# Performance work log

Measured on AMD Instinct MI355X. Metric: run time of the kernel, lower is better.

## Reference

```python
import jax, jax.numpy as jnp
import numpy as np

WH, WW, NUM_HEADS = 7, 7, 16
DIM = 512
B_WINDOWS = 4096   # batch * num_windows
NW = 64            # num_windows per image (mask groups)
N = WH * WW        # 49 tokens per window


def _relative_position_index():
    # Mirrors the torch buffer construction exactly (torch.meshgrid default is 'ij').
    coords = np.stack(np.meshgrid(np.arange(WH), np.arange(WW), indexing='ij'))  # [2,WH,WW]
    cf = coords.reshape(2, -1)                              # [2, N]
    rel = cf[:, :, None] - cf[:, None, :]                   # [2, N, N]
    rel = rel.transpose(1, 2, 0).copy()                     # [N, N, 2]
    rel[:, :, 0] += WH - 1
    rel[:, :, 1] += WW - 1
    rel[:, :, 0] *= 2 * WW - 1
    return jnp.asarray(rel.sum(-1), dtype=jnp.int32)        # [N, N]

REL_IDX = _relative_position_index()


def setup_inputs() -> dict:
    key = jax.random.key(0)
    ks = jax.random.split(key, 7)
    return {
        'x':          jax.random.normal(ks[0], (B_WINDOWS, N, DIM), jnp.float32),
        'mask':       jax.random.normal(ks[1], (NW, N, N), jnp.float32),
        'Wqkv':       jax.random.normal(ks[2], (3 * DIM, DIM), jnp.float32) * (DIM ** -0.5),
        'bqkv':       jax.random.normal(ks[3], (3 * DIM,), jnp.float32) * 0.02,
        'bias_table': jax.random.normal(ks[4], ((2 * WH - 1) * (2 * WW - 1), NUM_HEADS), jnp.float32) * 0.02,
        'Wproj':      jax.random.normal(ks[5], (DIM, DIM), jnp.float32) * (DIM ** -0.5),
        'bproj':      jax.random.normal(ks[6], (DIM,), jnp.float32) * 0.02,
    }


def reference(x, mask, Wqkv, bqkv, bias_table, Wproj, bproj):
    B, n, C = x.shape                      # [B_, 49, 512]
    hd = C // NUM_HEADS
    scale = hd ** -0.5
    qkv = (x @ Wqkv.T + bqkv).reshape(B, n, 3, NUM_HEADS, hd)
    qkv = qkv.transpose(2, 0, 3, 1, 4)     # [3, B, H, N, hd]
    q, k, v = qkv[0] * scale, qkv[1], qkv[2]
    attn = jnp.einsum('bhnd,bhmd->bhnm', q, k)          # [B, H, N, N]
    # gathered relative position bias: [1, H, N, N]
    bias = bias_table[REL_IDX].transpose(2, 0, 1)[None]
    attn = attn + bias
    nW = mask.shape[0]
    attn = attn.reshape(B // nW, nW, NUM_HEADS, n, n) + mask[None, :, None]
    attn = jax.nn.softmax(attn.reshape(B, NUM_HEADS, n, n), axis=-1)
    out = jnp.einsum('bhnm,bhmd->bhnd', attn, v)        # [B, H, N, hd]
    out = out.transpose(0, 2, 1, 3).reshape(B, n, C)
    return out @ Wproj.T + bproj
```

## Files before the change

kernel.cpp:

```cpp
#include <hip/hip_runtime.h>
#include <stdint.h>

#define NHEADS 16
#define DIM 512
#define BWIN 4096
#define NTOK 49
#define M_TOTAL (BWIN * NTOK)
#define QSCALE 0.17677669529663687f

typedef __attribute__((ext_vector_type(4)))  float f32x4;
typedef __attribute__((ext_vector_type(16))) float f32x16;
typedef __attribute__((ext_vector_type(8)))  short s16x8;
typedef __attribute__((ext_vector_type(4)))  short s16x4;

__device__ __forceinline__ f32x4 mfma16(s16x8 a, s16x8 b, f32x4 c) {
    return __builtin_amdgcn_mfma_f32_16x16x32_bf16(a, b, c, 0, 0, 0);
}
__device__ __forceinline__ f32x16 mfma32(s16x8 a, s16x8 b, f32x16 c) {
    return __builtin_amdgcn_mfma_f32_32x32x16_bf16(a, b, c, 0, 0, 0);
}

__device__ __forceinline__ short f2bf(float f) {
    unsigned u = __builtin_bit_cast(unsigned, f);
    u += 0x7FFFu + ((u >> 16) & 1u);
    return (short)(u >> 16);
}

__device__ __forceinline__ unsigned cvtpk(float a, float b) {
    unsigned r;
    asm("v_cvt_pk_bf16_f32 %0, %1, %2" : "=v"(r) : "v"(a), "v"(b));
    return r;
}

__device__ __forceinline__ void gload16(const void* g, void* l) {
    __builtin_amdgcn_global_load_lds(
        (const __attribute__((address_space(1))) void*)g,
        (__attribute__((address_space(3))) void*)l, 16, 0, 0);
}


__global__ void k_prep_x(const float* __restrict__ x, short* __restrict__ xb) {
    int i = blockIdx.x * blockDim.x + threadIdx.x;
    int stride = gridDim.x * blockDim.x;
    const int n4 = M_TOTAL * DIM / 4;
    for (; i < n4; i += stride) {
        f32x4 v = ((const f32x4*)x)[i];
        s16x4 o;
        o[0] = f2bf(v[0]); o[1] = f2bf(v[1]); o[2] = f2bf(v[2]); o[3] = f2bf(v[3]);
        ((s16x4*)xb)[i] = o;
    }
}

__global__ void k_prep_w(const float* __restrict__ src, short* __restrict__ dst,
                         int n, int scale_lim) {
    int i = blockIdx.x * blockDim.x + threadIdx.x;
    int stride = gridDim.x * blockDim.x;
    for (; i < n; i += stride) {
        float v = src[i];
        if (i < scale_lim) v *= QSCALE;
        dst[i] = f2bf(v);
    }
}

__global__ void k_prep_bm(const float* __restrict__ btab, const float* __restrict__ mask,
                          float* __restrict__ bmT) {
    int idx = blockIdx.x * blockDim.x + threadIdx.x;
    int stride = gridDim.x * blockDim.x;
    const int n = 64 * NHEADS * 49 * 64;
    for (; idx < n; idx += stride) {
        int i = idx & 63;
        int rest = idx >> 6;
        int j = rest % 49;
        int wh = rest / 49;
        int head = wh & 15;
        int w64 = wh >> 4;
        float v = 0.f;
        if (i < 49) {
            int ridx = (i / 7 - j / 7 + 6) * 13 + (i % 7 - j % 7 + 6);
            v = btab[ridx * 16 + head] + mask[(w64 * 49 + i) * 49 + j];
        }
        bmT[idx] = v;
    }
}

template <int MODE>
__global__ __launch_bounds__(512, 2) void k_gemm(
    const short* __restrict__ A, const short* __restrict__ B,
    const float* __restrict__ bias, void* __restrict__ C,
    int ntiles, int nwg) {
    __shared__ short lA[2][256 * 64];
    __shared__ short lB[2][256 * 64];
    const int K = 512;
    const size_t MP = M_TOTAL;

    int bid   = blockIdx.x;
    int chunk = nwg >> 3;
    int wg    = (bid & 7) * chunk + (bid >> 3);
    int mt = wg / ntiles;
    int nt = wg - mt * ntiles;

    int t = threadIdx.x;
    int lane = t & 63, wid = t >> 6;
    int l15 = lane & 15, g = (lane >> 4) & 3;
    int wr = wid >> 2, wc = wid & 3;

    const short* aT = A + (size_t)mt * 256 * K;
    const short* bT = B + (size_t)nt * 256 * K;

    f32x4 acc[8][4] = {};
    s16x8 af[4][2], bf0[2][2], bf1[2][2];

#define STAGE_A(buf, H, kt) do {                                               \
    _Pragma("unroll") for (int j = 0; j < 2; j++) {                            \
        int r_ = j * 128 + (H) * 64 + (t >> 3);                                \
        int sc_ = (t & 7) ^ (r_ & 7);                                          \
        gload16(aT + (size_t)r_ * K + (kt) * 64 + sc_ * 8,                     \
                &lA[buf][r_ * 64 + (t & 7) * 8]);                              \
    } } while (0)

#define STAGE_B(buf, H, kt) do {                                               \
    _Pragma("unroll") for (int j = 0; j < 2; j++) {                            \
        int u_ = j * 64 + (t >> 3);                                            \
        int r_ = ((u_ >> 5) << 6) | ((H) << 5) | (u_ & 31);                    \
        int sc_ = (t & 7) ^ (r_ & 7);                                          \
        gload16(bT + (size_t)r_ * K + (kt) * 64 + sc_ * 8,                     \
                &lB[buf][r_ * 64 + (t & 7) * 8]);                              \
    } } while (0)

#define LDA(MH, cur) do {                                                      \
    const short* pa_ = &lA[cur][(wr * 128 + (MH) * 64 + l15) * 64];            \
    _Pragma("unroll") for (int mi = 0; mi < 4; mi++)                           \
    _Pragma("unroll") for (int ks = 0; ks < 2; ks++)                           \
        af[mi][ks] = *(const s16x8*)(pa_ + mi * 1024 +                         \
                                     (((ks * 4 + g) ^ (l15 & 7)) * 8));        \
    } while (0)

#define LDB(BF, NH, cur) do {                                                  \
    const short* pb_ = &lB[cur][(wc * 64 + (NH) * 32 + l15) * 64];             \
    _Pragma("unroll") for (int nj = 0; nj < 2; nj++)                           \
    _Pragma("unroll") for (int ks = 0; ks < 2; ks++)                           \
        BF[nj][ks] = *(const s16x8*)(pb_ + nj * 1024 +                         \
                                     (((ks * 4 + g) ^ (l15 & 7)) * 8));        \
    } while (0)

#define MMQ(BF, MH, NH) do {                                                   \
    __builtin_amdgcn_s_setprio(1);                                             \
    _Pragma("unroll") for (int ks = 0; ks < 2; ks++)                           \
    _Pragma("unroll") for (int mi = 0; mi < 4; mi++)                           \
    _Pragma("unroll") for (int nj = 0; nj < 2; nj++)                           \
        acc[(MH) * 4 + mi][(NH) * 2 + nj] =                                    \
            mfma16(af[mi][ks], BF[nj][ks], acc[(MH) * 4 + mi][(NH) * 2 + nj]); \
    __builtin_amdgcn_s_setprio(0);                                             \
} while (0)

#define BAR() __builtin_amdgcn_s_barrier()
#define LGW() do { asm volatile("s_waitcnt lgkmcnt(0)" ::: "memory");          \
                   __builtin_amdgcn_sched_barrier(0); } while (0)
#define VMW(st) do {                                                           \
    if (st) asm volatile("s_waitcnt vmcnt(4)" ::: "memory");                   \
    else    asm volatile("s_waitcnt vmcnt(0)" ::: "memory"); } while (0)

    STAGE_A(0, 0, 0);
    STAGE_B(0, 0, 0);
    STAGE_B(0, 1, 0);
    STAGE_A(0, 1, 0);
    asm volatile("s_waitcnt vmcnt(4)" ::: "memory");
    BAR();

    for (int kt = 0; kt < 8; ++kt) {
        const int cur = kt & 1, nxt = cur ^ 1;
        const bool st = kt < 7;
        LDA(0, cur); LDB(bf0, 0, cur);
        if (st) STAGE_A(nxt, 0, kt + 1);
        VMW(st); BAR(); LGW();
        MMQ(bf0, 0, 0);
        BAR();
        LDB(bf1, 1, cur);
        if (st) STAGE_B(nxt, 0, kt + 1);
        VMW(st); BAR(); LGW();
        MMQ(bf1, 0, 1);
        BAR();
        LDA(1, cur);
        if (st) STAGE_B(nxt, 1, kt + 1);
        VMW(st); BAR(); LGW();
        MMQ(bf1, 1, 1);
        BAR();
        if (st) STAGE_A(nxt, 1, kt + 1);
        VMW(st); BAR(); LGW();
        MMQ(bf0, 1, 0);
        BAR();
    }

#undef STAGE_A
#undef STAGE_B
#undef LDA
#undef LDB
#undef MMQ
#undef BAR
#undef LGW
#undef VMW

    int m0 = mt * 256 + wr * 128;
    int n0 = nt * 256 + wc * 64;

    if (MODE == 0) {
        short* region = (wid < 4) ? (&lA[0][0] + wid * 8192)
                                  : (&lB[0][0] + (wid - 4) * 8192);
#pragma unroll
        for (int a = 0; a < 4; a++) {
            int co = (a >> 1) * 32 + (a & 1) * 16;
            int n = n0 + co + l15;
            float bv = bias[n];
            if (n < 512) bv *= QSCALE;
            int w16 = (co >> 3) + (l15 >> 3);
#pragma unroll
            for (int mi = 0; mi < 8; mi++)
#pragma unroll
                for (int r = 0; r < 4; r++) {
                    int row = mi * 16 + g * 4 + r;
                    region[row * 64 + ((w16 ^ (row & 7)) * 8) + (l15 & 7)] =
                        f2bf(acc[mi][a][r] + bv);
                }
        }
#pragma unroll
        for (int p = 0; p < 2; p++) {
            int plane = (n0 >> 5) + p;
            short* dst = (short*)C + ((size_t)plane * MP + m0) * 32;
#pragma unroll
            for (int i = 0; i < 8; i++) {
                int f = i * 64 + lane;
                int row = f >> 2, c = f & 3;
                s16x8 v = *(const s16x8*)(region + row * 64 +
                                          (((p * 4 + c) ^ (row & 7)) * 8));
                *(s16x8*)(dst + (size_t)f * 8) = v;
            }
        }
    } else {
#pragma unroll
        for (int a = 0; a < 4; a++) {
            int co = (a >> 1) * 32 + (a & 1) * 16;
            int n = n0 + co + l15;
            float bv = bias[n];
#pragma unroll
            for (int mi = 0; mi < 8; mi++)
#pragma unroll
                for (int r = 0; r < 4; r++) {
                    int m = m0 + mi * 16 + g * 4 + r;
                    ((float*)C)[(size_t)m * 512 + n] = acc[mi][a][r] + bv;
                }
        }
    }
}

__global__ __launch_bounds__(256, 4) void k_attn(
    const short* __restrict__ qkv, const float* __restrict__ bmT,
    short* __restrict__ ao) {
    int wid = threadIdx.x >> 6, lane = threadIdx.x & 63;
    int p = blockIdx.x * 4 + wid;
    int w = p >> 4, head = p & 15;
    int l31 = lane & 31, h = lane >> 5;
    const size_t MP = M_TOTAL;

    const short* qb = qkv + ((size_t)head * MP + w * 49) * 32;
    const short* kb = qb + (size_t)16 * MP * 32;
    const short* vb = qb + (size_t)32 * MP * 32;

    s16x8 qf[2][2], kf[2][2];
#pragma unroll
    for (int t = 0; t < 2; t++) {
        int row = t * 32 + l31;
#pragma unroll
        for (int s = 0; s < 2; s++) {
            qf[t][s] = *(const s16x8*)(qb + row * 32 + 16 * s + 8 * h);
            kf[t][s] = *(const s16x8*)(kb + row * 32 + 16 * s + 8 * h);
        }
    }

    union U8 { short s[8]; s16x8 v; };
    U8 vf[4];
#pragma unroll
    for (int jc = 0; jc < 4; jc++)
#pragma unroll
        for (int e = 0; e < 8; e++)
            vf[jc].s[e] = vb[(16 * jc + 8 * h + e) * 32 + l31];

    f32x16 st[2][2] = {};
#pragma unroll
    for (int s = 0; s < 2; s++)
#pragma unroll
        for (int jt = 0; jt < 2; jt++)
#pragma unroll
            for (int it = 0; it < 2; it++)
                st[jt][it] = mfma32(kf[jt][s], qf[it][s], st[jt][it]);

    const float* bs = bmT + ((size_t)((w & 63) * NHEADS + head)) * 3136 + l31;
#pragma unroll
    for (int jt = 0; jt < 2; jt++)
#pragma unroll
        for (int it = 0; it < 2; it++)
#pragma unroll
            for (int r = 0; r < 16; r++) {
                int j = 32 * jt + (r & 3) + 8 * (r >> 2) + 4 * h;
                if (j < 49) st[jt][it][r] += bs[j * 64 + 32 * it];
                else        st[jt][it][r] = -1e30f;
            }

    float inv[2];
#pragma unroll
    for (int it = 0; it < 2; it++) {
        float mx = -1e30f;
#pragma unroll
        for (int jt = 0; jt < 2; jt++)
#pragma unroll
            for (int r = 0; r < 16; r++) mx = fmaxf(mx, st[jt][it][r]);
        mx = fmaxf(mx, __shfl_xor(mx, 32));
        float sum = 0.f;
#pragma unroll
        for (int jt = 0; jt < 2; jt++)
#pragma unroll
            for (int r = 0; r < 16; r++) {
                float e = __expf(st[jt][it][r] - mx);
                st[jt][it][r] = e;
                sum += e;
            }
        sum += __shfl_xor(sum, 32);
        inv[it] = 1.0f / sum;
    }

    f32x16 oacc[2] = {};
#pragma unroll
    for (int jc = 0; jc < 4; jc++) {
        const int jt = jc >> 1, rb = 8 * (jc & 1);
#pragma unroll
        for (int it = 0; it < 2; it++) {
            float iv = inv[it];
            unsigned pk0  = cvtpk(st[jt][it][rb + 0] * iv, st[jt][it][rb + 1] * iv);
            unsigned pk0b = cvtpk(st[jt][it][rb + 2] * iv, st[jt][it][rb + 3] * iv);
            unsigned pk1  = cvtpk(st[jt][it][rb + 4] * iv, st[jt][it][rb + 5] * iv);
            unsigned pk1b = cvtpk(st[jt][it][rb + 6] * iv, st[jt][it][rb + 7] * iv);
            unsigned o0  = __shfl_xor(pk0, 32);
            unsigned o0b = __shfl_xor(pk0b, 32);
            unsigned o1  = __shfl_xor(pk1, 32);
            unsigned o1b = __shfl_xor(pk1b, 32);
            union { unsigned d[4]; s16x8 v; } pa;
            pa.d[0] = h ? o1  : pk0;
            pa.d[1] = h ? o1b : pk0b;
            pa.d[2] = h ? pk1 : o0;
            pa.d[3] = h ? pk1b : o0b;
            oacc[it] = mfma32(pa.v, vf[jc].v, oacc[it]);
        }
    }

    short* ob = ao + (size_t)w * 49 * 512 + head * 32 + l31;
#pragma unroll
    for (int it = 0; it < 2; it++)
#pragma unroll
        for (int r = 0; r < 16; r++) {
            int i = 32 * it + 4 * h + (r & 3) + 8 * (r >> 2);
            if (i < 49) ob[(size_t)i * 512] = f2bf(oacc[it][r]);
        }
}


extern "C" void kernel_launch(void* const* d_in, const int* in_sizes, int n_in,
                              void* d_out, int out_size, void* d_ws, size_t ws_size,
                              hipStream_t stream) {
    const float* x     = (const float*)d_in[0];
    const float* mask  = (const float*)d_in[1];
    const float* Wqkv  = (const float*)d_in[2];
    const float* bqkv  = (const float*)d_in[3];
    const float* btab  = (const float*)d_in[4];
    const float* Wproj = (const float*)d_in[5];
    const float* bproj = (const float*)d_in[6];
    float* out = (float*)d_out;

    char* ws = (char*)d_ws;
    size_t off = 0;
    short* xb     = (short*)(ws + off); off += (size_t)M_TOTAL * 512 * 2;
    short* qkvb   = (short*)(ws + off); off += (size_t)48 * M_TOTAL * 32 * 2 + 65536;
    short* Wqkvb  = (short*)(ws + off); off += (size_t)1536 * 512 * 2;
    short* Wprojb = (short*)(ws + off); off += (size_t)512 * 512 * 2;
    float* bmT    = (float*)(ws + off); off += (size_t)64 * NHEADS * 49 * 64 * 4;
    short* ao = xb;

    k_prep_x<<<2048, 256, 0, stream>>>(x, xb);
    k_prep_w<<<1536, 256, 0, stream>>>(Wqkv, Wqkvb, 1536 * 512, 512 * 512);
    k_prep_w<<<512, 256, 0, stream>>>(Wproj, Wprojb, 512 * 512, 0);
    k_prep_bm<<<2048, 256, 0, stream>>>(btab, mask, bmT);

    k_gemm<0><<<4704, 512, 0, stream>>>(xb, Wqkvb, bqkv, qkvb, 6, 4704);
    k_attn<<<16384, 256, 0, stream>>>(qkvb, bmT, ao);
    k_gemm<1><<<1568, 512, 0, stream>>>(ao, Wprojb, bproj, out, 2, 1568);
}
```

Before: 1.164 ms.

## Deepen GEMM global-to-LDS prefetch pipeline and peel final k-iteration

Restructures the double-buffered K loop so the A half-tile for iteration kt+2 is staged into the current buffer after its last use, keeping more global loads in flight (vmcnt 6 instead of 4). The last iteration is peeled into an epilogue with progressively draining waits, which removes the per-iteration conditional staging. This aims to hide more global memory latency behind MFMA work, at the cost of more complex buffer-reuse ordering and more outstanding loads.

```diff
diff --git a/kernel.cpp b/kernel.cpp
--- a/kernel.cpp
+++ b/kernel.cpp
@@ -156,37 +156,57 @@
 #define BAR() __builtin_amdgcn_s_barrier()
 #define LGW() do { asm volatile("s_waitcnt lgkmcnt(0)" ::: "memory");          \
                    __builtin_amdgcn_sched_barrier(0); } while (0)
-#define VMW(st) do {                                                           \
-    if (st) asm volatile("s_waitcnt vmcnt(4)" ::: "memory");                   \
-    else    asm volatile("s_waitcnt vmcnt(0)" ::: "memory"); } while (0)
+#define VMW(n) asm volatile("s_waitcnt vmcnt(" #n ")" ::: "memory")
 
     STAGE_A(0, 0, 0);
     STAGE_B(0, 0, 0);
     STAGE_B(0, 1, 0);
     STAGE_A(0, 1, 0);
-    asm volatile("s_waitcnt vmcnt(4)" ::: "memory");
+    STAGE_A(1, 0, 1);
+    VMW(6);
     BAR();
 
-    for (int kt = 0; kt < 8; ++kt) {
+    for (int kt = 0; kt < 7; ++kt) {
         const int cur = kt & 1, nxt = cur ^ 1;
-        const bool st = kt < 7;
         LDA(0, cur); LDB(bf0, 0, cur);
-        if (st) STAGE_A(nxt, 0, kt + 1);
-        VMW(st); BAR(); LGW();
+        STAGE_B(nxt, 0, kt + 1);
+        VMW(6); BAR(); LGW();
         MMQ(bf0, 0, 0);
         BAR();
         LDB(bf1, 1, cur);
-        if (st) STAGE_B(nxt, 0, kt + 1);
-        VMW(st); BAR(); LGW();
+        STAGE_B(nxt, 1, kt + 1);
+        VMW(6); BAR(); LGW();
         MMQ(bf1, 0, 1);
         BAR();
         LDA(1, cur);
-        if (st) STAGE_B(nxt, 1, kt + 1);
-        VMW(st); BAR(); LGW();
+        STAGE_A(nxt, 1, kt + 1);
+        VMW(6); BAR(); LGW();
         MMQ(bf1, 1, 1);
         BAR();
-        if (st) STAGE_A(nxt, 1, kt + 1);
-        VMW(st); BAR(); LGW();
+        if (kt < 6) {
+            STAGE_A(cur, 0, kt + 2);
+            VMW(6);
+        } else {
+            VMW(4);
+        }
+        BAR(); LGW();
+        MMQ(bf0, 1, 0);
+        BAR();
+    }
+    {
+        LDA(0, 1); LDB(bf0, 0, 1);
+        VMW(2); BAR(); LGW();
+        MMQ(bf0, 0, 0);
+        BAR();
+        LDB(bf1, 1, 1);
+        VMW(0); BAR(); LGW();
+        MMQ(bf1, 0, 1);
+        BAR();
+        LDA(1, 1);
+        BAR(); LGW();
+        MMQ(bf1, 1, 1);
+        BAR();
+        LGW();
         MMQ(bf0, 1, 0);
         BAR();
     }
```

After: 1.174 ms. No clear change (+0.9%).

## Double-buffer A fragments and prefetch next tile's A from LDS during MFMA

Applied to the files above, without the earlier changes.

Reworks the GEMM main loop so it keeps two register sets of A fragments and a single B fragment set. The next k-tile's A fragments are read from LDS while the current MFMAs run, using partial lgkmcnt waits (lgkmcnt(8)) instead of full drains. Global-to-LDS staging is regrouped, with explicit vmcnt counts tuned to the new issue order. The aim is to hide LDS read latency behind matrix work. In exchange it uses more registers, reloads the B fragments an extra time per iteration, and depends on hand-counted wait values being correct.

```diff
diff --git a/kernel.cpp b/kernel.cpp
--- a/kernel.cpp
+++ b/kernel.cpp
@@ -108,7 +108,7 @@
     const short* bT = B + (size_t)nt * 256 * K;
 
     f32x4 acc[8][4] = {};
-    s16x8 af[4][2], bf0[2][2], bf1[2][2];
+    s16x8 afA[4][2], afB[4][2], S[2][2];
 
 #define STAGE_A(buf, H, kt) do {                                               \
     _Pragma("unroll") for (int j = 0; j < 2; j++) {                            \
@@ -127,77 +127,90 @@
                 &lB[buf][r_ * 64 + (t & 7) * 8]);                              \
     } } while (0)
 
-#define LDA(MH, cur) do {                                                      \
-    const short* pa_ = &lA[cur][(wr * 128 + (MH) * 64 + l15) * 64];            \
+#define LDAF(DST, MH, buf) do {                                                \
+    const short* pa_ = &lA[buf][(wr * 128 + (MH) * 64 + l15) * 64];            \
     _Pragma("unroll") for (int mi = 0; mi < 4; mi++)                           \
     _Pragma("unroll") for (int ks = 0; ks < 2; ks++)                           \
-        af[mi][ks] = *(const s16x8*)(pa_ + mi * 1024 +                         \
-                                     (((ks * 4 + g) ^ (l15 & 7)) * 8));        \
+        DST[mi][ks] = *(const s16x8*)(pa_ + mi * 1024 +                        \
+                                      (((ks * 4 + g) ^ (l15 & 7)) * 8));       \
     } while (0)
 
-#define LDB(BF, NH, cur) do {                                                  \
-    const short* pb_ = &lB[cur][(wc * 64 + (NH) * 32 + l15) * 64];             \
+#define LDBS(NH, buf) do {                                                     \
+    const short* pb_ = &lB[buf][(wc * 64 + (NH) * 32 + l15) * 64];             \
     _Pragma("unroll") for (int nj = 0; nj < 2; nj++)                           \
     _Pragma("unroll") for (int ks = 0; ks < 2; ks++)                           \
-        BF[nj][ks] = *(const s16x8*)(pb_ + nj * 1024 +                         \
-                                     (((ks * 4 + g) ^ (l15 & 7)) * 8));        \
+        S[nj][ks] = *(const s16x8*)(pb_ + nj * 1024 +                          \
+                                    (((ks * 4 + g) ^ (l15 & 7)) * 8));         \
     } while (0)
 
-#define MMQ(BF, MH, NH) do {                                                   \
+#define MMQ2(ASET, MH, NH) do {                                                \
     __builtin_amdgcn_s_setprio(1);                                             \
     _Pragma("unroll") for (int ks = 0; ks < 2; ks++)                           \
     _Pragma("unroll") for (int mi = 0; mi < 4; mi++)                           \
     _Pragma("unroll") for (int nj = 0; nj < 2; nj++)                           \
         acc[(MH) * 4 + mi][(NH) * 2 + nj] =                                    \
-            mfma16(af[mi][ks], BF[nj][ks], acc[(MH) * 4 + mi][(NH) * 2 + nj]); \
+            mfma16(ASET[mi][ks], S[nj][ks], acc[(MH) * 4 + mi][(NH) * 2 + nj]);\
     __builtin_amdgcn_s_setprio(0);                                             \
 } while (0)
 
 #define BAR() __builtin_amdgcn_s_barrier()
-#define LGW() do { asm volatile("s_waitcnt lgkmcnt(0)" ::: "memory");          \
-                   __builtin_amdgcn_sched_barrier(0); } while (0)
-#define VMW(st) do {                                                           \
-    if (st) asm volatile("s_waitcnt vmcnt(4)" ::: "memory");                   \
-    else    asm volatile("s_waitcnt vmcnt(0)" ::: "memory"); } while (0)
+#define SB0() __builtin_amdgcn_sched_barrier(0)
+#define LGK0 do { asm volatile("s_waitcnt lgkmcnt(0)" ::: "memory"); SB0(); } while (0)
+#define LGK8 do { asm volatile("s_waitcnt lgkmcnt(8)" ::: "memory"); SB0(); } while (0)
+#define VMW(n) asm volatile("s_waitcnt vmcnt(" #n ")" ::: "memory")
 
     STAGE_A(0, 0, 0);
     STAGE_B(0, 0, 0);
     STAGE_B(0, 1, 0);
     STAGE_A(0, 1, 0);
-    asm volatile("s_waitcnt vmcnt(4)" ::: "memory");
+    VMW(6);
     BAR();
+    LDAF(afA, 0, 0);
 
     for (int kt = 0; kt < 8; ++kt) {
         const int cur = kt & 1, nxt = cur ^ 1;
         const bool st = kt < 7;
-        LDA(0, cur); LDB(bf0, 0, cur);
-        if (st) STAGE_A(nxt, 0, kt + 1);
-        VMW(st); BAR(); LGW();
-        MMQ(bf0, 0, 0);
-        BAR();
-        LDB(bf1, 1, cur);
-        if (st) STAGE_B(nxt, 0, kt + 1);
-        VMW(st); BAR(); LGW();
-        MMQ(bf1, 0, 1);
-        BAR();
-        LDA(1, cur);
-        if (st) STAGE_B(nxt, 1, kt + 1);
-        VMW(st); BAR(); LGW();
-        MMQ(bf1, 1, 1);
+        if (st) { STAGE_A(nxt, 0, kt + 1); STAGE_B(nxt, 0, kt + 1); VMW(6); }
+        else VMW(2);
+        BAR();
+        LDBS(0, cur);
+        LGK0;
+        MMQ2(afA, 0, 0);
+        BAR();
+        if (st) { STAGE_B(nxt, 1, kt + 1); VMW(6); }
+        else VMW(0);
+        BAR();
+        LDBS(1, cur);
+        SB0();
+        LDAF(afB, 1, cur);
+        LGK8;
+        MMQ2(afA, 0, 1);
         BAR();
         if (st) STAGE_A(nxt, 1, kt + 1);
-        VMW(st); BAR(); LGW();
-        MMQ(bf0, 1, 0);
+        BAR();
+        LGK0;
+        MMQ2(afB, 1, 1);
+        BAR();
+        if (st) VMW(6);
+        BAR();
+        LDBS(0, cur);
+        if (st) {
+            SB0();
+            LDAF(afA, 0, nxt);
+            LGK8;
+        } else {
+            LGK0;
+        }
+        MMQ2(afB, 1, 0);
         BAR();
     }
 
 #undef STAGE_A
 #undef STAGE_B
-#undef LDA
-#undef LDB
-#undef MMQ
-#undef BAR
-#undef LGW
+#undef LDAF
+#undef LDBS
+#undef MMQ2
+#undef SB0
 #undef VMW
 
     int m0 = mt * 256 + wr * 128;
```

New measurement: 1.280 ms. 1.1x slower.
